# Optimization experiments

Measured on AMD Instinct MI355X. Metric: run time of the kernel, lower is better.

## Reference

```python
import jax, jax.numpy as jnp
import numpy as np

B, L, D_MODEL, D_K = 4, 2048, 1024, 128


def setup_inputs() -> dict:
    key = jax.random.key(0)
    ks = jax.random.split(key, 4)
    scale = 1.0 / np.sqrt(D_MODEL)
    x = jax.random.normal(ks[0], (B, L, D_MODEL), dtype=jnp.float32)
    Wq = jax.random.normal(ks[1], (D_MODEL, D_K), dtype=jnp.float32) * scale
    Wk = jax.random.normal(ks[2], (D_MODEL, D_K), dtype=jnp.float32) * scale
    Wv = jax.random.normal(ks[3], (D_MODEL, D_K), dtype=jnp.float32) * scale
    bq = jnp.zeros((D_K,), dtype=jnp.float32)
    bk = jnp.zeros((D_K,), dtype=jnp.float32)
    bv = jnp.zeros((D_K,), dtype=jnp.float32)
    return {"x": x, "Wq": Wq, "bq": bq, "Wk": Wk, "bk": bk, "Wv": Wv, "bv": bv}


def reference(x, Wq, bq, Wk, bk, Wv, bv):
    # Dense projections (keras Dense = xW + b)
    Q = jnp.einsum("bld,dk->blk", x, Wq) + bq  # [B, L, d_k]
    K = jnp.einsum("bld,dk->blk", x, Wk) + bk
    V = jnp.einsum("bld,dk->blk", x, Wv) + bv
    QK = jnp.einsum("blk,bmk->blm", Q, K)      # [B, L, L]
    # Original: real( complex(cos(QK), sin(QK)) @ complex(V, 0) )
    # Since imag(V) == 0, the real part is exactly cos(QK) @ V; the sin
    # branch contributes only to the discarded imaginary part.
    out = jnp.einsum("blm,bmk->blk", jnp.cos(QK), V)  # [B, L, d_k]
    return out
```

## Files before the change

kernel.cpp:

```cpp
#include <hip/hip_runtime.h>

typedef _Float16 half8_t __attribute__((ext_vector_type(8)));
typedef __attribute__((ext_vector_type(4))) float float4_t;

#define MFMA16 __builtin_amdgcn_mfma_f32_16x16x32_f16

constexpr int BB   = 4;
constexpr int LL   = 2048;
constexpr int DM   = 1024;
constexpr int DK   = 128;
constexpr int MTOT = BB * LL;
constexpr int MC   = 4;
constexpr float INV2PI = 0.15915494309189535f;


__device__ __forceinline__ void gload16(const void* g, void* l) {
    __builtin_amdgcn_global_load_lds(
        (const __attribute__((address_space(1))) void*)g,
        (__attribute__((address_space(3))) void*)l, 16, 0, 0);
}

__global__ __launch_bounds__(256) void k0_wsplit(
        const float* __restrict__ wq, const float* __restrict__ wk,
        const float* __restrict__ wv,
        _Float16* __restrict__ wq6, _Float16* __restrict__ wk6,
        _Float16* __restrict__ wv6) {
    int kc = blockIdx.x, a = blockIdx.y;
    const float* w = (a == 0) ? wq : (a == 1) ? wk : wv;
    _Float16* dst = (a == 0) ? wq6 : (a == 1) ? wk6 : wv6;
    __shared__ float tile[64 * 132];
    int t = threadIdx.x;
#pragma unroll
    for (int j = 0; j < 8; ++j) {
        int idx4 = t + j * 256;
        int kr = idx4 >> 5, n4 = idx4 & 31;
        *(float4_t*)(&tile[kr * 132 + n4 * 4]) =
            *(const float4_t*)(w + (size_t)(kc * 64 + kr) * DK + n4 * 4);
    }
    __syncthreads();
#pragma unroll
    for (int sw = 0; sw < 4; ++sw) {
        int ch = t + sw * 256;
        int cbt = ch >> 7, s = (ch >> 4) & 7, cc = ch & 15;
        int kb = (s >> 2) * 32 + (s & 3) * 8;
        int n = cbt * 16 + cc;
        half8_t h;
#pragma unroll
        for (int e = 0; e < 8; ++e) h[e] = (_Float16)tile[(kb + e) * 132 + n];
        *(half8_t*)(dst + (size_t)kc * 8192 + ch * 8) = h;
    }
}

__global__ __launch_bounds__(256, 3) void k1_proj(
        const float* __restrict__ x,
        const float* __restrict__ bq, const float* __restrict__ bk,
        const float* __restrict__ bv,
        const _Float16* __restrict__ wq6, const _Float16* __restrict__ wk6,
        const _Float16* __restrict__ wv6,
        _Float16* __restrict__ qim, _Float16* __restrict__ kim,
        _Float16* __restrict__ vim) {
    int mt = blockIdx.x, grp = blockIdx.y;
    int rowbase = mt * 32;
    __shared__ __attribute__((aligned(16))) _Float16 xs[2][32 * 72];
    __shared__ __attribute__((aligned(16))) _Float16 wsm[2][8192];

    int t = threadIdx.x, lane = t & 63, wid = t >> 6;
    int cc = lane & 15, g = lane >> 4;
    const _Float16* W6 = (grp == 0) ? wq6 : (grp == 1) ? wk6 : wv6;

    float4_t acc[2][2];
#pragma unroll
    for (int rf = 0; rf < 2; ++rf)
#pragma unroll
        for (int cf = 0; cf < 2; ++cf) acc[rf][cf] = (float4_t){0.f, 0.f, 0.f, 0.f};

    int xr = t >> 3, xc8 = t & 7;
    const float* xsrc = x + (size_t)(rowbase + xr) * DM + xc8 * 8;
    int xoff = xr * 72 + xc8 * 8;

    auto stageW = [&](int kc, int buf) {
        const _Float16* Wp = W6 + (size_t)kc * 8192;
#pragma unroll
        for (int i = 0; i < 4; ++i)
            gload16(Wp + i * 2048 + t * 8, (char*)wsm[buf] + i * 4096 + wid * 1024);
    };
    auto cvt8 = [&](float4_t f0, float4_t f1) {
        half8_t h;
#pragma unroll
        for (int e = 0; e < 4; ++e) { h[e] = (_Float16)f0[e]; h[e + 4] = (_Float16)f1[e]; }
        return h;
    };

    {
        float4_t f0 = *(const float4_t*)(xsrc);
        float4_t f1 = *(const float4_t*)(xsrc + 4);
        stageW(0, 0);
        *(half8_t*)(xs[0] + xoff) = cvt8(f0, f1);
    }
    __syncthreads();

#pragma unroll 1
    for (int kc = 0; kc < 16; ++kc) {
        int cb = kc & 1, nb = cb ^ 1;
        bool more = (kc < 15);
        float4_t f0, f1;
        if (more) {
            f0 = *(const float4_t*)(xsrc + (size_t)(kc + 1) * 64);
            f1 = *(const float4_t*)(xsrc + (size_t)(kc + 1) * 64 + 4);
            stageW(kc + 1, nb);
        }
        half8_t a_[2][2], b_[2][2];
#pragma unroll
        for (int rf = 0; rf < 2; ++rf)
#pragma unroll
            for (int ks = 0; ks < 2; ++ks)
                a_[rf][ks] = *(const half8_t*)(xs[cb] + (rf * 16 + cc) * 72 + ks * 32 + g * 8);
#pragma unroll
        for (int cf = 0; cf < 2; ++cf)
#pragma unroll
            for (int ks = 0; ks < 2; ++ks)
                b_[cf][ks] = *(const half8_t*)(wsm[cb] + (wid * 2 + cf) * 1024 +
                                               (ks * 4 + g) * 128 + cc * 8);
#pragma unroll
        for (int cf = 0; cf < 2; ++cf)
#pragma unroll
            for (int rf = 0; rf < 2; ++rf) {
                acc[rf][cf] = MFMA16(a_[rf][0], b_[cf][0], acc[rf][cf], 0, 0, 0);
                acc[rf][cf] = MFMA16(a_[rf][1], b_[cf][1], acc[rf][cf], 0, 0, 0);
            }
        if (more) *(half8_t*)(xs[nb] + xoff) = cvt8(f0, f1);
        __syncthreads();
    }

    const float* bias = (grp == 0) ? bq : (grp == 1) ? bk : bv;
#pragma unroll
    for (int rf = 0; rf < 2; ++rf)
#pragma unroll
        for (int cf = 0; cf < 2; ++cf) {
            int c = wid * 32 + cf * 16 + cc;
            float bv_ = bias[c];
#pragma unroll
            for (int i = 0; i < 4; ++i) {
                int r = rowbase + rf * 16 + g * 4 + i;
                float v = acc[rf][cf][i] + bv_;
                if (grp == 0) {
                    size_t o = (size_t)(r >> 4) * 2048 + (c >> 5) * 512 +
                               ((c >> 3) & 3) * 128 + (r & 15) * 8 + (c & 7);
                    qim[o] = (_Float16)v;
                } else if (grp == 1) {
                    size_t o = (size_t)(r >> 5) * 4096 + ((r >> 4) & 1) * 2048 +
                               (c >> 5) * 512 + ((c >> 3) & 3) * 128 +
                               (r & 15) * 8 + (c & 7);
                    kim[o] = (_Float16)v;
                } else {
                    size_t o = (size_t)(r >> 5) * 4096 + (c >> 4) * 512 +
                               ((r >> 3) & 3) * 128 + (c & 15) * 8 + (r & 7);
                    vim[o] = (_Float16)v;
                }
            }
        }
}

__global__ __launch_bounds__(256, 2) void k2_attn(
        const _Float16* __restrict__ qim, const _Float16* __restrict__ kim,
        const _Float16* __restrict__ vim, float* __restrict__ part) {
    int mc = blockIdx.x, qt = blockIdx.y, b = blockIdx.z;
    int t = threadIdx.x, lane = t & 63, wid = t >> 6;
    int cc = lane & 15, g = lane >> 4;

    __shared__ __attribute__((aligned(16))) _Float16 kb[2][8192];
    __shared__ __attribute__((aligned(16))) _Float16 vb[2][8192];
    __shared__ __attribute__((aligned(16))) _Float16 ps[4][1024];

    int qrow = b * LL + qt * 64 + wid * 16;
    const _Float16* qb_ = qim + (size_t)(qrow >> 4) * 2048;
    half8_t qf[4];
#pragma unroll
    for (int s = 0; s < 4; ++s)
        qf[s] = *(const half8_t*)(qb_ + s * 512 + g * 128 + cc * 8);

    float4_t o[8];
#pragma unroll
    for (int cf = 0; cf < 8; ++cf) o[cf] = (float4_t){0.f, 0.f, 0.f, 0.f};

    int tbase = b * 64 + mc * 16;

    auto stageKV = [&](int mi, int buf) {
        const _Float16* ks = kim + (size_t)(tbase + mi * 2) * 4096;
        const _Float16* vs = vim + (size_t)(tbase + mi * 2) * 4096;
#pragma unroll
        for (int i = 0; i < 4; ++i) {
            gload16(ks + i * 2048 + t * 8, (char*)kb[buf] + i * 4096 + wid * 1024);
            gload16(vs + i * 2048 + t * 8, (char*)vb[buf] + i * 4096 + wid * 1024);
        }
    };

    stageKV(0, 0);
    __syncthreads();

#pragma unroll 1
    for (int mi = 0; mi < 8; ++mi) {
        int cb = mi & 1, nb = cb ^ 1;
        if (mi < 7) stageKV(mi + 1, nb);
        float4_t sa[4];
#pragma unroll
        for (int cf = 0; cf < 4; ++cf) sa[cf] = (float4_t){0.f, 0.f, 0.f, 0.f};
#pragma unroll
        for (int cf = 0; cf < 4; ++cf)
#pragma unroll
            for (int s = 0; s < 4; ++s) {
                half8_t bh = *(const half8_t*)(kb[cb] + cf * 2048 + s * 512 +
                                               g * 128 + cc * 8);
                sa[cf] = MFMA16(qf[s], bh, sa[cf], 0, 0, 0);
            }
#pragma unroll
        for (int cf = 0; cf < 4; ++cf)
#pragma unroll
            for (int i = 0; i < 4; ++i) {
                float rv = sa[cf][i] * INV2PI;
                rv = rv - floorf(rv);
                float cv;
                asm volatile("v_cos_f32 %0, %1" : "=v"(cv) : "v"(rv));
                int m = cf * 16 + cc, q = g * 4 + i;
                ps[wid][(m >> 3) * 128 + q * 8 + (m & 7)] = (_Float16)cv;
            }
#pragma unroll
        for (int ksv = 0; ksv < 2; ++ksv) {
            half8_t pa = *(const half8_t*)(&ps[wid][(ksv * 4 + g) * 128 + cc * 8]);
#pragma unroll
            for (int cf = 0; cf < 8; ++cf) {
                half8_t vbf = *(const half8_t*)(vb[cb] + ksv * 4096 + cf * 512 +
                                                g * 128 + cc * 8);
                o[cf] = MFMA16(pa, vbf, o[cf], 0, 0, 0);
            }
        }
        __syncthreads();
    }
    float* pp = part + ((size_t)(mc * BB + b) * LL + qt * 64 + wid * 16) * DK;
#pragma unroll
    for (int cf = 0; cf < 8; ++cf)
#pragma unroll
        for (int i = 0; i < 4; ++i)
            pp[(g * 4 + i) * DK + cf * 16 + cc] = o[cf][i];
}

__global__ __launch_bounds__(256) void k3_reduce(const float4_t* __restrict__ part,
                                                 float4_t* __restrict__ out) {
    constexpr int NT4 = MTOT * DK / 4;
    int idx = blockIdx.x * 256 + threadIdx.x;
    float4_t s = part[idx];
#pragma unroll
    for (int c = 1; c < MC; ++c) s += part[idx + (size_t)c * NT4];
    out[idx] = s;
}

extern "C" void kernel_launch(void* const* d_in, const int* in_sizes, int n_in,
                              void* d_out, int out_size, void* d_ws, size_t ws_size,
                              hipStream_t stream) {
    const float* x  = (const float*)d_in[0];
    const float* Wq = (const float*)d_in[1];
    const float* bq = (const float*)d_in[2];
    const float* Wk = (const float*)d_in[3];
    const float* bk = (const float*)d_in[4];
    const float* Wv = (const float*)d_in[5];
    const float* bv = (const float*)d_in[6];

    char* ws = (char*)d_ws;
    size_t off = 0;
    auto alloc = [&](size_t bytes) -> char* {
        char* p = ws + off;
        off += (bytes + 255) & ~(size_t)255;
        return p;
    };
    _Float16* wq6 = (_Float16*)alloc((size_t)DK * DM * 2);
    _Float16* wk6 = (_Float16*)alloc((size_t)DK * DM * 2);
    _Float16* wv6 = (_Float16*)alloc((size_t)DK * DM * 2);
    _Float16* qim = (_Float16*)alloc((size_t)MTOT * DK * 2);
    _Float16* kim = (_Float16*)alloc((size_t)MTOT * DK * 2);
    _Float16* vim = (_Float16*)alloc((size_t)MTOT * DK * 2);
    float* part = (float*)alloc((size_t)MC * MTOT * DK * 4);

    k0_wsplit<<<dim3(16, 3), 256, 0, stream>>>(Wq, Wk, Wv, wq6, wk6, wv6);
    k1_proj<<<dim3(MTOT / 32, 3), 256, 0, stream>>>(x, bq, bk, bv,
                                                    wq6, wk6, wv6, qim, kim, vim);
    k2_attn<<<dim3(MC, LL / 64, BB), 256, 0, stream>>>(qim, kim, vim, part);
    k3_reduce<<<(MTOT * DK / 4) / 256, 256, 0, stream>>>((const float4_t*)part,
                                                         (float4_t*)d_out);
}
```

Before: 49.45 us.

## Store split-K partials in fp16 and vectorize cos-score LDS writes

The attention kernel now writes its per-chunk partial outputs as fp16 instead of fp32, which halves the partial buffer traffic in both the attention store and the reduce kernel. The reduce kernel reads half8 vectors and accumulates in fp32. Separately, the QK MFMA operands are swapped so each lane holds transposed scores, letting the cos results be packed into one half4 LDS store instead of scattered scalar stores. Rounding partial sums to fp16 adds precision loss.

```diff
diff --git a/kernel.cpp b/kernel.cpp
--- a/kernel.cpp
+++ b/kernel.cpp
@@ -1,6 +1,7 @@
 #include <hip/hip_runtime.h>
 
 typedef _Float16 half8_t __attribute__((ext_vector_type(8)));
+typedef _Float16 half4_t __attribute__((ext_vector_type(4)));
 typedef __attribute__((ext_vector_type(4))) float float4_t;
 
 #define MFMA16 __builtin_amdgcn_mfma_f32_16x16x32_f16
@@ -12,7 +13,6 @@
 constexpr int MTOT = BB * LL;
 constexpr int MC   = 4;
 constexpr float INV2PI = 0.15915494309189535f;
-
 
 __device__ __forceinline__ void gload16(const void* g, void* l) {
     __builtin_amdgcn_global_load_lds(
@@ -163,7 +163,7 @@
 
 __global__ __launch_bounds__(256, 2) void k2_attn(
         const _Float16* __restrict__ qim, const _Float16* __restrict__ kim,
-        const _Float16* __restrict__ vim, float* __restrict__ part) {
+        const _Float16* __restrict__ vim, _Float16* __restrict__ part) {
     int mc = blockIdx.x, qt = blockIdx.y, b = blockIdx.z;
     int t = threadIdx.x, lane = t & 63, wid = t >> 6;
     int cc = lane & 15, g = lane >> 4;
@@ -209,21 +209,24 @@
         for (int cf = 0; cf < 4; ++cf)
 #pragma unroll
             for (int s = 0; s < 4; ++s) {
-                half8_t bh = *(const half8_t*)(kb[cb] + cf * 2048 + s * 512 +
+                half8_t kf = *(const half8_t*)(kb[cb] + cf * 2048 + s * 512 +
                                                g * 128 + cc * 8);
-                sa[cf] = MFMA16(qf[s], bh, sa[cf], 0, 0, 0);
-            }
-#pragma unroll
-        for (int cf = 0; cf < 4; ++cf)
+                sa[cf] = MFMA16(kf, qf[s], sa[cf], 0, 0, 0);
+            }
+#pragma unroll
+        for (int cf = 0; cf < 4; ++cf) {
+            half4_t h4;
 #pragma unroll
             for (int i = 0; i < 4; ++i) {
                 float rv = sa[cf][i] * INV2PI;
                 rv = rv - floorf(rv);
                 float cv;
                 asm volatile("v_cos_f32 %0, %1" : "=v"(cv) : "v"(rv));
-                int m = cf * 16 + cc, q = g * 4 + i;
-                ps[wid][(m >> 3) * 128 + q * 8 + (m & 7)] = (_Float16)cv;
-            }
+                h4[i] = (_Float16)cv;
+            }
+            int base = (cf * 2 + (g >> 1)) * 128 + cc * 8 + (g & 1) * 4;
+            *(half4_t*)(&ps[wid][base]) = h4;
+        }
 #pragma unroll
         for (int ksv = 0; ksv < 2; ++ksv) {
             half8_t pa = *(const half8_t*)(&ps[wid][(ksv * 4 + g) * 128 + cc * 8]);
@@ -236,22 +239,32 @@
         }
         __syncthreads();
     }
-    float* pp = part + ((size_t)(mc * BB + b) * LL + qt * 64 + wid * 16) * DK;
+    _Float16* pp = part + ((size_t)(mc * BB + b) * LL + qt * 64 + wid * 16) * DK;
 #pragma unroll
     for (int cf = 0; cf < 8; ++cf)
 #pragma unroll
         for (int i = 0; i < 4; ++i)
-            pp[(g * 4 + i) * DK + cf * 16 + cc] = o[cf][i];
-}
-
-__global__ __launch_bounds__(256) void k3_reduce(const float4_t* __restrict__ part,
+            pp[(g * 4 + i) * DK + cf * 16 + cc] = (_Float16)o[cf][i];
+}
+
+__global__ __launch_bounds__(256) void k3_reduce(const _Float16* __restrict__ part,
                                                  float4_t* __restrict__ out) {
-    constexpr int NT4 = MTOT * DK / 4;
+    constexpr int NT8 = MTOT * DK / 8;
     int idx = blockIdx.x * 256 + threadIdx.x;
-    float4_t s = part[idx];
-#pragma unroll
-    for (int c = 1; c < MC; ++c) s += part[idx + (size_t)c * NT4];
-    out[idx] = s;
+    const half8_t* p = (const half8_t*)part;
+    float s[8];
+#pragma unroll
+    for (int e = 0; e < 8; ++e) s[e] = 0.f;
+#pragma unroll
+    for (int c = 0; c < MC; ++c) {
+        half8_t v = p[idx + (size_t)c * NT8];
+#pragma unroll
+        for (int e = 0; e < 8; ++e) s[e] += (float)v[e];
+    }
+    float4_t o0 = {s[0], s[1], s[2], s[3]};
+    float4_t o1 = {s[4], s[5], s[6], s[7]};
+    out[idx * 2]     = o0;
+    out[idx * 2 + 1] = o1;
 }
 
 extern "C" void kernel_launch(void* const* d_in, const int* in_sizes, int n_in,
@@ -278,12 +291,11 @@
     _Float16* qim = (_Float16*)alloc((size_t)MTOT * DK * 2);
     _Float16* kim = (_Float16*)alloc((size_t)MTOT * DK * 2);
     _Float16* vim = (_Float16*)alloc((size_t)MTOT * DK * 2);
-    float* part = (float*)alloc((size_t)MC * MTOT * DK * 4);
+    _Float16* part = (_Float16*)alloc((size_t)MC * MTOT * DK * 2);
 
     k0_wsplit<<<dim3(16, 3), 256, 0, stream>>>(Wq, Wk, Wv, wq6, wk6, wv6);
     k1_proj<<<dim3(MTOT / 32, 3), 256, 0, stream>>>(x, bq, bk, bv,
                                                     wq6, wk6, wv6, qim, kim, vim);
     k2_attn<<<dim3(MC, LL / 64, BB), 256, 0, stream>>>(qim, kim, vim, part);
-    k3_reduce<<<(MTOT * DK / 4) / 256, 256, 0, stream>>>((const float4_t*)part,
-                                                         (float4_t*)d_out);
-}
+    k3_reduce<<<(MTOT * DK / 8) / 256, 256, 0, stream>>>(part, (float4_t*)d_out);
+}
```

Measured after the change: 47.41 us, median of 2. -4.1%, faster.
